# Kernel optimization log

Hardware: AMD Instinct MI355X
Metric: run time of the kernel (lower is better)

The kernel has to match this reference:

```python
import jax, jax.numpy as jnp
import numpy as np

N_NODES = 50000
N_EDGES = 800000
NFEAT = 256
NHID = 512
BN_EPS = 1e-5


def setup_inputs() -> dict:
    key = jax.random.key(0)
    ks = jax.random.split(key, 6)
    x = jax.random.normal(ks[0], (N_NODES, NFEAT), dtype=jnp.float32)
    edge_index = jax.random.randint(ks[1], (2, N_EDGES), 0, N_NODES, dtype=jnp.int64)
    # Xavier-uniform linear weights, zero biases (matches weights_init)
    lim1 = np.sqrt(6.0 / (NFEAT + NHID))
    W1 = jax.random.uniform(ks[2], (NFEAT, NHID), minval=-lim1, maxval=lim1, dtype=jnp.float32)
    b1 = jnp.zeros((NHID,), dtype=jnp.float32)
    lim2 = np.sqrt(6.0 / (NHID + NHID))
    W2 = jax.random.uniform(ks[3], (NHID, NHID), minval=-lim2, maxval=lim2, dtype=jnp.float32)
    b2 = jnp.zeros((NHID,), dtype=jnp.float32)
    gamma = jnp.ones((NHID,), dtype=jnp.float32)
    beta = jnp.zeros((NHID,), dtype=jnp.float32)
    return {"x": x, "edge_index": edge_index, "W1": W1, "b1": b1,
            "gamma": gamma, "beta": beta, "W2": W2, "b2": b2}


def reference(x, edge_index, W1, b1, gamma, beta, W2, b2):
    # GINConv (eps=0): h_i = MLP(x_i + sum_{j->i} x_j)
    src = edge_index[0]
    dst = edge_index[1]
    agg = jax.ops.segment_sum(x[src], dst, num_segments=x.shape[0])  # [N, nfeat]
    h = x + agg
    # MLP: Linear -> ReLU -> BatchNorm1d (training-mode batch stats) -> Linear
    h = jax.nn.relu(h @ W1 + b1)  # [N, nhid]
    mean = jnp.mean(h, axis=0)
    var = jnp.var(h, axis=0)  # biased, as PyTorch uses for normalization
    h = (h - mean) * jax.lax.rsqrt(var + BN_EPS) * gamma + beta
    return h @ W2 + b2
```

## Files before the change

kernel.cpp:

```cpp
#include <hip/hip_runtime.h>

#define NNODES 50000
#define NF 256
#define NH 512
#define MPAD 50048
#define NRB 391
#define BN_EPS 1e-5f
#define NSCAN 196

typedef unsigned short u16;
typedef __attribute__((ext_vector_type(8))) short bf16x8;
typedef __attribute__((ext_vector_type(4))) float f32x4;

__device__ __forceinline__ float bf2f(u16 u) {
  union { unsigned int i; float f; } v; v.i = ((unsigned int)u) << 16; return v.f;
}
__device__ __forceinline__ u16 f2bf(float f) {
  union { float ff; unsigned int i; } v; v.ff = f;
  unsigned int r = v.i + 0x7FFFu + ((v.i >> 16) & 1u);
  return (u16)(r >> 16);
}

__device__ __forceinline__ void async16(const void* g, void* l) {
  __builtin_amdgcn_global_load_lds(
      (const __attribute__((address_space(1))) unsigned int*)g,
      (__attribute__((address_space(3))) unsigned int*)l, 16, 0, 0);
}

__global__ __launch_bounds__(256) void conv_tr_kernel(const float* __restrict__ x,
                                                      u16* __restrict__ xbf,
                                                      const float* __restrict__ W1,
                                                      u16* __restrict__ W1t) {
  const int b = blockIdx.x;
  if (b < 2048) {
    const size_t n8 = (size_t)NNODES * NF / 8;
    size_t stride = (size_t)2048 * 256;
    for (size_t i = b * (size_t)256 + threadIdx.x; i < n8; i += stride) {
      float4 a = ((const float4*)x)[2 * i];
      float4 c = ((const float4*)x)[2 * i + 1];
      ushort4 lo, hi;
      lo.x = f2bf(a.x); lo.y = f2bf(a.y); lo.z = f2bf(a.z); lo.w = f2bf(a.w);
      hi.x = f2bf(c.x); hi.y = f2bf(c.y); hi.z = f2bf(c.z); hi.w = f2bf(c.w);
      ((ushort4*)xbf)[2 * i] = lo;
      ((ushort4*)xbf)[2 * i + 1] = hi;
    }
  } else {
    int idx = (b - 2048) * 256 + threadIdx.x;
    int n = idx >> 8;
    int k = idx & 255;
    W1t[(size_t)n * NF + k] = f2bf(W1[(size_t)k * NH + n]);
  }
}

__global__ __launch_bounds__(256) void hist_kernel(const int* __restrict__ ei,
                                                   int* __restrict__ deg, int E) {
  __shared__ int sf;
  if (threadIdx.x < 64) {
    unsigned long long bb = __ballot(ei[2 * threadIdx.x + 1] == 0);
    if (threadIdx.x == 0) sf = (bb == ~0ull) ? 1 : 0;
  }
  __syncthreads();
  const int is64 = sf;
  const int gtid = blockIdx.x * 256 + threadIdx.x;
  const int stride = gridDim.x * 256;
  if (is64) {
    const int4* d4 = (const int4*)(ei + 2 * (size_t)E);
    int np = E >> 1;
    for (int p = gtid; p < np; p += stride) {
      int4 d = d4[p];
      if ((unsigned)d.x < NNODES) atomicAdd(&deg[d.x], 1);
      if ((unsigned)d.z < NNODES) atomicAdd(&deg[d.z], 1);
    }
    for (int e = (np << 1) + gtid; e < E; e += stride) {
      int d = ei[2 * (size_t)E + 2 * e];
      if ((unsigned)d < NNODES) atomicAdd(&deg[d], 1);
    }
  } else {
    const int4* d4 = (const int4*)(ei + E);
    int np = E >> 2;
    for (int p = gtid; p < np; p += stride) {
      int4 d = d4[p];
      if ((unsigned)d.x < NNODES) atomicAdd(&deg[d.x], 1);
      if ((unsigned)d.y < NNODES) atomicAdd(&deg[d.y], 1);
      if ((unsigned)d.z < NNODES) atomicAdd(&deg[d.z], 1);
      if ((unsigned)d.w < NNODES) atomicAdd(&deg[d.w], 1);
    }
    for (int e = (np << 2) + gtid; e < E; e += stride) {
      int d = ei[(size_t)E + e];
      if ((unsigned)d < NNODES) atomicAdd(&deg[d], 1);
    }
  }
}

__global__ __launch_bounds__(256) void scan_a(const int* __restrict__ deg,
                                              int* __restrict__ rowptr,
                                              int* __restrict__ blocksums) {
  const int t = threadIdx.x;
  int i = blockIdx.x * 256 + t;
  int v = (i < NNODES) ? deg[i] : 0;
  __shared__ int sm[256];
  sm[t] = v;
  __syncthreads();
  for (int off = 1; off < 256; off <<= 1) {
    int u = (t >= off) ? sm[t - off] : 0;
    __syncthreads();
    sm[t] += u;
    __syncthreads();
  }
  if (i < NNODES) rowptr[i] = sm[t] - v;
  if (t == 255) blocksums[blockIdx.x] = sm[255];
}

__global__ __launch_bounds__(256) void scan_b(const int* __restrict__ blocksums,
                                              int* __restrict__ rowptr,
                                              int* __restrict__ cw) {
  const int t = threadIdx.x;
  __shared__ int sm[256];
  sm[t] = (t < NSCAN) ? blocksums[t] : 0;
  __syncthreads();
  for (int off = 1; off < 256; off <<= 1) {
    int u = (t >= off) ? sm[t - off] : 0;
    __syncthreads();
    sm[t] += u;
    __syncthreads();
  }
  const int boff = (blockIdx.x == 0) ? 0 : sm[blockIdx.x - 1];
  int i = blockIdx.x * 256 + t;
  if (i < NNODES) {
    int rv = rowptr[i] + boff;
    rowptr[i] = rv;
    cw[i] = rv;
  }
  if (blockIdx.x == 0 && t == 0) rowptr[NNODES] = sm[NSCAN - 1];
}

__global__ __launch_bounds__(256) void fill_kernel(const int* __restrict__ ei, int E,
                                                   int* __restrict__ cw,
                                                   int* __restrict__ srcs) {
  __shared__ int sf;
  if (threadIdx.x < 64) {
    unsigned long long bb = __ballot(ei[2 * threadIdx.x + 1] == 0);
    if (threadIdx.x == 0) sf = (bb == ~0ull) ? 1 : 0;
  }
  __syncthreads();
  const int is64 = sf;
  const int gtid = blockIdx.x * 256 + threadIdx.x;
  const int stride = gridDim.x * 256;
  if (is64) {
    const int4* s4 = (const int4*)ei;
    const int4* d4 = (const int4*)(ei + 2 * (size_t)E);
    int np = E >> 1;
    for (int p = gtid; p < np; p += stride) {
      int4 sv = s4[p], dv = d4[p];
      if ((unsigned)sv.x < NNODES && (unsigned)dv.x < NNODES) {
        int pos = atomicAdd(&cw[dv.x], 1);
        if ((unsigned)pos < (unsigned)E) srcs[pos] = sv.x;
      }
      if ((unsigned)sv.z < NNODES && (unsigned)dv.z < NNODES) {
        int pos = atomicAdd(&cw[dv.z], 1);
        if ((unsigned)pos < (unsigned)E) srcs[pos] = sv.z;
      }
    }
    for (int e = (np << 1) + gtid; e < E; e += stride) {
      int src = ei[2 * e], dst = ei[2 * (size_t)E + 2 * e];
      if ((unsigned)src >= NNODES || (unsigned)dst >= NNODES) continue;
      int pos = atomicAdd(&cw[dst], 1);
      if ((unsigned)pos < (unsigned)E) srcs[pos] = src;
    }
  } else {
    const int4* s4 = (const int4*)ei;
    const int4* d4 = (const int4*)(ei + E);
    int np = E >> 2;
    for (int p = gtid; p < np; p += stride) {
      int4 sv = s4[p], dv = d4[p];
      int ss[4] = {sv.x, sv.y, sv.z, sv.w};
      int dd[4] = {dv.x, dv.y, dv.z, dv.w};
#pragma unroll
      for (int j = 0; j < 4; ++j) {
        if ((unsigned)ss[j] < NNODES && (unsigned)dd[j] < NNODES) {
          int pos = atomicAdd(&cw[dd[j]], 1);
          if ((unsigned)pos < (unsigned)E) srcs[pos] = ss[j];
        }
      }
    }
    for (int e = (np << 2) + gtid; e < E; e += stride) {
      int src = ei[e], dst = ei[(size_t)E + e];
      if ((unsigned)src >= NNODES || (unsigned)dst >= NNODES) continue;
      int pos = atomicAdd(&cw[dst], 1);
      if ((unsigned)pos < (unsigned)E) srcs[pos] = src;
    }
  }
}

__global__ __launch_bounds__(256) void gather_kernel(const u16* __restrict__ xbf,
                                                     const int* __restrict__ srcs,
                                                     const int* __restrict__ rowptr,
                                                     u16* __restrict__ hpad) {
  const int hl = threadIdx.x & 31;
  const int node = blockIdx.x * 8 + (threadIdx.x >> 5);
  if (node >= MPAD) return;
  bf16x8* outp = (bf16x8*)(hpad + (size_t)node * NF + hl * 8);
  if (node >= NNODES) {
    bf16x8 z = {0, 0, 0, 0, 0, 0, 0, 0};
    *outp = z;
    return;
  }
  bf16x8 sv = *(const bf16x8*)(xbf + (size_t)node * NF + hl * 8);
  float acc[8];
#pragma unroll
  for (int j = 0; j < 8; ++j) acc[j] = bf2f((u16)sv[j]);
  int e = rowptr[node];
  const int e1 = rowptr[node + 1];
  for (; e + 7 < e1; e += 8) {
    bf16x8 v[8];
#pragma unroll
    for (int u = 0; u < 8; ++u)
      v[u] = *(const bf16x8*)(xbf + (size_t)srcs[e + u] * NF + hl * 8);
#pragma unroll
    for (int u = 0; u < 8; ++u)
#pragma unroll
      for (int j = 0; j < 8; ++j) acc[j] += bf2f((u16)v[u][j]);
  }
  for (; e + 3 < e1; e += 4) {
    bf16x8 v[4];
#pragma unroll
    for (int u = 0; u < 4; ++u)
      v[u] = *(const bf16x8*)(xbf + (size_t)srcs[e + u] * NF + hl * 8);
#pragma unroll
    for (int u = 0; u < 4; ++u)
#pragma unroll
      for (int j = 0; j < 8; ++j) acc[j] += bf2f((u16)v[u][j]);
  }
  for (; e < e1; ++e) {
    bf16x8 v0 = *(const bf16x8*)(xbf + (size_t)srcs[e] * NF + hl * 8);
#pragma unroll
    for (int j = 0; j < 8; ++j) acc[j] += bf2f((u16)v0[j]);
  }
  bf16x8 o;
#pragma unroll
  for (int j = 0; j < 8; ++j) o[j] = (short)f2bf(acc[j]);
  *outp = o;
}

template <int K, bool RELU, bool OUTF32, bool STATS>
__global__ __launch_bounds__(256) void gemm_bt(const u16* __restrict__ Ab,
                                               const u16* __restrict__ Bt,
                                               const float* __restrict__ bias,
                                               void* __restrict__ Cp, int Mstore,
                                               float* __restrict__ parts) {
  __shared__ __align__(16) u16 As[128 * 64];
  __shared__ __align__(16) u16 Bs[128 * 64];
  __shared__ float sred[256];
  const int tid = threadIdx.x;
  const int lane = tid & 63;
  const int wid = tid >> 6;
  const int wr = wid >> 1, wc = wid & 1;

  const int nwg = gridDim.x;
  const int q = nwg >> 3, r = nwg & 7;
  const int xcd = blockIdx.x & 7, idx = blockIdx.x >> 3;
  const int work = (xcd < r ? xcd * (q + 1) : r * (q + 1) + (xcd - r) * q) + idx;
  const int brow = (work >> 2) * 128;
  const int bcol = (work & 3) * 128;

  f32x4 acc[4][4] = {};

  const int lrow = lane >> 3;
  const int lkc = ((lane & 7) ^ (lrow & 7)) * 8;
  const int nt = K / 64;

  if (STATS) {
    if (tid < 64) ((float4*)sred)[tid] = (float4){0.f, 0.f, 0.f, 0.f};
  }

  for (int t = 0; t < nt; ++t) {
    const int k0 = t * 64;
#pragma unroll
    for (int i = 0; i < 4; ++i) {
      int c = i * 4 + wid;
      int row = c * 8 + lrow;
      async16(Ab + (size_t)(brow + row) * K + k0 + lkc, &As[c * 512]);
      async16(Bt + (size_t)(bcol + row) * K + k0 + lkc, &Bs[c * 512]);
    }
    __syncthreads();
#pragma unroll
    for (int ks = 0; ks < 2; ++ks) {
      bf16x8 af[4], bfr[4];
      const int rchunk = ((ks << 2) + (lane >> 4)) ^ (lane & 7);
#pragma unroll
      for (int m = 0; m < 4; ++m)
        af[m] = *(const bf16x8*)&As[(wr * 64 + m * 16 + (lane & 15)) * 64 + rchunk * 8];
#pragma unroll
      for (int n = 0; n < 4; ++n)
        bfr[n] = *(const bf16x8*)&Bs[(wc * 64 + n * 16 + (lane & 15)) * 64 + rchunk * 8];
#pragma unroll
      for (int n = 0; n < 4; ++n)
#pragma unroll
        for (int m = 0; m < 4; ++m)
          acc[n][m] = __builtin_amdgcn_mfma_f32_16x16x32_bf16(bfr[n], af[m], acc[n][m], 0, 0, 0);
    }
    __syncthreads();
  }

  const int row_base = brow + wr * 64 + (lane & 15);
  const int col_base = bcol + wc * 64 + ((lane >> 4) << 2);
#pragma unroll
  for (int n = 0; n < 4; ++n) {
    int col = col_base + n * 16;
    float4 bv4 = *(const float4*)&bias[col];
    float s0 = 0.f, s1 = 0.f, s2 = 0.f, s3 = 0.f;
    float q0 = 0.f, q1 = 0.f, q2 = 0.f, q3 = 0.f;
#pragma unroll
    for (int m = 0; m < 4; ++m) {
      int row = row_base + m * 16;
      f32x4 a = acc[n][m];
      float v0 = a[0] + bv4.x, v1 = a[1] + bv4.y, v2 = a[2] + bv4.z, v3 = a[3] + bv4.w;
      if (RELU) {
        v0 = fmaxf(v0, 0.f); v1 = fmaxf(v1, 0.f);
        v2 = fmaxf(v2, 0.f); v3 = fmaxf(v3, 0.f);
      }
      if (row < Mstore) {
        if (OUTF32) {
          float4 o = {v0, v1, v2, v3};
          *(float4*)&((float*)Cp)[(size_t)row * NH + col] = o;
        } else {
          ushort4 o = {f2bf(v0), f2bf(v1), f2bf(v2), f2bf(v3)};
          *(ushort4*)&((u16*)Cp)[(size_t)row * NH + col] = o;
        }
      }
      if (STATS && row < NNODES) {
        s0 += v0; s1 += v1; s2 += v2; s3 += v3;
        q0 += v0 * v0; q1 += v1 * v1; q2 += v2 * v2; q3 += v3 * v3;
      }
    }
    if (STATS) {
#pragma unroll
      for (int msk = 1; msk < 16; msk <<= 1) {
        s0 += __shfl_xor(s0, msk); s1 += __shfl_xor(s1, msk);
        s2 += __shfl_xor(s2, msk); s3 += __shfl_xor(s3, msk);
        q0 += __shfl_xor(q0, msk); q1 += __shfl_xor(q1, msk);
        q2 += __shfl_xor(q2, msk); q3 += __shfl_xor(q3, msk);
      }
      if ((lane & 15) == 0) {
        int lc = wc * 64 + n * 16 + ((lane >> 4) << 2);
        atomicAdd(&sred[lc + 0], s0); atomicAdd(&sred[lc + 1], s1);
        atomicAdd(&sred[lc + 2], s2); atomicAdd(&sred[lc + 3], s3);
        atomicAdd(&sred[128 + lc + 0], q0); atomicAdd(&sred[128 + lc + 1], q1);
        atomicAdd(&sred[128 + lc + 2], q2); atomicAdd(&sred[128 + lc + 3], q3);
      }
    }
  }
  if (STATS) {
    __syncthreads();
    if (tid < 128) {
      parts[(size_t)work * 256 + tid] = sred[tid];
      parts[(size_t)work * 256 + 128 + tid] = sred[128 + tid];
    }
  }
}

__global__ __launch_bounds__(256) void stats_bn(const float* __restrict__ parts,
                                                const float* __restrict__ gamma,
                                                const float* __restrict__ beta,
                                                float* __restrict__ a_arr,
                                                float* __restrict__ c_arr,
                                                int* __restrict__ err) {
  int c = blockIdx.x * 256 + threadIdx.x;
  int grp = (c >> 7) & 3, cl = c & 127;
  float s = 0.f, qq = 0.f;
  for (int rb = 0; rb < NRB; ++rb) {
    const float* p = parts + (size_t)((rb << 2) + grp) * 256 + cl;
    s += p[0];
    qq += p[128];
  }
  float mean = s * (1.f / NNODES);
  float var = qq * (1.f / NNODES) - mean * mean;
  if (!(mean == mean) || !(var == var) ||
      fabsf(mean) > 1e20f || var > 1e20f || var < -1e-2f)
    err[0] = 2;
  if (var < 0.f) var = 0.f;
  float a = gamma[c] * rsqrtf(var + BN_EPS);
  a_arr[c] = a;
  c_arr[c] = beta[c] - mean * a;
}

__global__ __launch_bounds__(256) void fold_w2(const float* __restrict__ W2,
                                               const float* __restrict__ b2,
                                               const float* __restrict__ a_arr,
                                               const float* __restrict__ c_arr,
                                               u16* __restrict__ W2pt,
                                               float* __restrict__ bias2p) {
  int n = blockIdx.x;
  int t = threadIdx.x;
  float accv = 0.f;
  for (int k = t; k < NH; k += 256) {
    float w = W2[(size_t)k * NH + n];
    W2pt[(size_t)n * NH + k] = f2bf(a_arr[k] * w);
    accv += c_arr[k] * w;
  }
  __shared__ float red[256];
  red[t] = accv;
  __syncthreads();
  for (int s = 128; s > 0; s >>= 1) {
    if (t < s) red[t] += red[t + s];
    __syncthreads();
  }
  if (t == 0) bias2p[n] = b2[n] + red[0];
}

__global__ __launch_bounds__(256) void write_sentinel(float* __restrict__ out, int n, float val) {
  int stride = gridDim.x * blockDim.x;
  for (int i = blockIdx.x * blockDim.x + threadIdx.x; i < n; i += stride) out[i] = val;
}

__global__ __launch_bounds__(256) void apply_err(const int* __restrict__ err,
                                                 float* __restrict__ out, int n) {
  if (err[0] == 0) return;
  int stride = gridDim.x * blockDim.x;
  for (int i = blockIdx.x * blockDim.x + threadIdx.x; i < n; i += stride) out[i] = -500000.f;
}

extern "C" void kernel_launch(void* const* d_in, const int* in_sizes, int n_in,
                              void* d_out, int out_size, void* d_ws, size_t ws_size,
                              hipStream_t stream) {
  const float* x     = (const float*)d_in[0];
  const int*   ei    = (const int*)d_in[1];
  const float* W1    = (const float*)d_in[2];
  const float* b1    = (const float*)d_in[3];
  const float* gamma = (const float*)d_in[4];
  const float* beta  = (const float*)d_in[5];
  const float* W2    = (const float*)d_in[6];
  const float* b2    = (const float*)d_in[7];
  float* out = (float*)d_out;
  const int E = in_sizes[1] / 2;

  char* ws = (char*)d_ws;
  size_t off = 0;
  auto alloc = [&](size_t bytes) {
    char* p = ws + off;
    off += (bytes + 255) & ~(size_t)255;
    return p;
  };
  u16*   xbf    = (u16*)alloc((size_t)NNODES * NF * 2);
  u16*   hpad   = (u16*)alloc((size_t)MPAD * NF * 2);
  u16*   h1     = (u16*)alloc((size_t)MPAD * NH * 2);
  u16*   W1t    = (u16*)alloc((size_t)NH * NF * 2);
  u16*   W2pt   = (u16*)alloc((size_t)NH * NH * 2);
  int*   srcs   = (int*)alloc((size_t)E * 4);
  int*   rowptr = (int*)alloc((size_t)(NNODES + 1) * 4);
  int*   cw     = (int*)alloc((size_t)NNODES * 4);
  int*   deg    = (int*)alloc((size_t)NNODES * 4);
  int*   bsums  = (int*)alloc(256 * 4);
  float* parts  = (float*)alloc((size_t)NRB * 4 * 256 * 4);
  int*   err    = (int*)alloc(8);
  float* a_arr  = (float*)alloc(NH * 4);
  float* c_arr  = (float*)alloc(NH * 4);
  float* bias2p = (float*)alloc(NH * 4);

  if (off > ws_size) {
    write_sentinel<<<2048, 256, 0, stream>>>(out, out_size,
        1.0e7f + 1048576.0f * (float)(ws_size >> 20));
    return;
  }

  hipMemsetAsync(deg, 0, (size_t)NNODES * 4, stream);
  hipMemsetAsync(err, 0, 8, stream);

  hist_kernel<<<1024, 256, 0, stream>>>(ei, deg, E);
  conv_tr_kernel<<<2560, 256, 0, stream>>>(x, xbf, W1, W1t);
  scan_a<<<NSCAN, 256, 0, stream>>>(deg, rowptr, bsums);
  scan_b<<<NSCAN, 256, 0, stream>>>(bsums, rowptr, cw);
  fill_kernel<<<1024, 256, 0, stream>>>(ei, E, cw, srcs);
  gather_kernel<<<MPAD / 8, 256, 0, stream>>>(xbf, srcs, rowptr, hpad);

  const int nwg = NRB * 4;
  gemm_bt<NF, true, false, true><<<nwg, 256, 0, stream>>>(hpad, W1t, b1, h1, MPAD, parts);

  stats_bn<<<2, 256, 0, stream>>>(parts, gamma, beta, a_arr, c_arr, err);
  fold_w2<<<NH, 256, 0, stream>>>(W2, b2, a_arr, c_arr, W2pt, bias2p);

  gemm_bt<NH, false, true, false><<<nwg, 256, 0, stream>>>(h1, W2pt, bias2p, out, NNODES, nullptr);

  apply_err<<<2048, 256, 0, stream>>>(err, out, out_size);
}
```

Before: 281.8 us.

## Replace CSR build with fixed-capacity per-node edge buckets

Removes the degree histogram and two prefix-scan kernels by scattering each edge source directly into a per-destination bucket of fixed capacity, with counts kept in the atomic cursor array. The gather kernel reads the bucket count and list directly instead of row pointers. This cuts several launches and one full pass over the edge list, at the cost of a larger, sparsely filled index buffer. An error flag is raised if any node exceeds the capacity.

```diff
diff --git a/kernel.cpp b/kernel.cpp
--- a/kernel.cpp
+++ b/kernel.cpp
@@ -6,7 +6,7 @@
 #define MPAD 50048
 #define NRB 391
 #define BN_EPS 1e-5f
-#define NSCAN 196
+#define CAP 96
 
 typedef unsigned short u16;
 typedef __attribute__((ext_vector_type(8))) short bf16x8;
@@ -52,91 +52,10 @@
   }
 }
 
-__global__ __launch_bounds__(256) void hist_kernel(const int* __restrict__ ei,
-                                                   int* __restrict__ deg, int E) {
-  __shared__ int sf;
-  if (threadIdx.x < 64) {
-    unsigned long long bb = __ballot(ei[2 * threadIdx.x + 1] == 0);
-    if (threadIdx.x == 0) sf = (bb == ~0ull) ? 1 : 0;
-  }
-  __syncthreads();
-  const int is64 = sf;
-  const int gtid = blockIdx.x * 256 + threadIdx.x;
-  const int stride = gridDim.x * 256;
-  if (is64) {
-    const int4* d4 = (const int4*)(ei + 2 * (size_t)E);
-    int np = E >> 1;
-    for (int p = gtid; p < np; p += stride) {
-      int4 d = d4[p];
-      if ((unsigned)d.x < NNODES) atomicAdd(&deg[d.x], 1);
-      if ((unsigned)d.z < NNODES) atomicAdd(&deg[d.z], 1);
-    }
-    for (int e = (np << 1) + gtid; e < E; e += stride) {
-      int d = ei[2 * (size_t)E + 2 * e];
-      if ((unsigned)d < NNODES) atomicAdd(&deg[d], 1);
-    }
-  } else {
-    const int4* d4 = (const int4*)(ei + E);
-    int np = E >> 2;
-    for (int p = gtid; p < np; p += stride) {
-      int4 d = d4[p];
-      if ((unsigned)d.x < NNODES) atomicAdd(&deg[d.x], 1);
-      if ((unsigned)d.y < NNODES) atomicAdd(&deg[d.y], 1);
-      if ((unsigned)d.z < NNODES) atomicAdd(&deg[d.z], 1);
-      if ((unsigned)d.w < NNODES) atomicAdd(&deg[d.w], 1);
-    }
-    for (int e = (np << 2) + gtid; e < E; e += stride) {
-      int d = ei[(size_t)E + e];
-      if ((unsigned)d < NNODES) atomicAdd(&deg[d], 1);
-    }
-  }
-}
-
-__global__ __launch_bounds__(256) void scan_a(const int* __restrict__ deg,
-                                              int* __restrict__ rowptr,
-                                              int* __restrict__ blocksums) {
-  const int t = threadIdx.x;
-  int i = blockIdx.x * 256 + t;
-  int v = (i < NNODES) ? deg[i] : 0;
-  __shared__ int sm[256];
-  sm[t] = v;
-  __syncthreads();
-  for (int off = 1; off < 256; off <<= 1) {
-    int u = (t >= off) ? sm[t - off] : 0;
-    __syncthreads();
-    sm[t] += u;
-    __syncthreads();
-  }
-  if (i < NNODES) rowptr[i] = sm[t] - v;
-  if (t == 255) blocksums[blockIdx.x] = sm[255];
-}
-
-__global__ __launch_bounds__(256) void scan_b(const int* __restrict__ blocksums,
-                                              int* __restrict__ rowptr,
-                                              int* __restrict__ cw) {
-  const int t = threadIdx.x;
-  __shared__ int sm[256];
-  sm[t] = (t < NSCAN) ? blocksums[t] : 0;
-  __syncthreads();
-  for (int off = 1; off < 256; off <<= 1) {
-    int u = (t >= off) ? sm[t - off] : 0;
-    __syncthreads();
-    sm[t] += u;
-    __syncthreads();
-  }
-  const int boff = (blockIdx.x == 0) ? 0 : sm[blockIdx.x - 1];
-  int i = blockIdx.x * 256 + t;
-  if (i < NNODES) {
-    int rv = rowptr[i] + boff;
-    rowptr[i] = rv;
-    cw[i] = rv;
-  }
-  if (blockIdx.x == 0 && t == 0) rowptr[NNODES] = sm[NSCAN - 1];
-}
-
-__global__ __launch_bounds__(256) void fill_kernel(const int* __restrict__ ei, int E,
+__global__ __launch_bounds__(256) void bucket_fill(const int* __restrict__ ei, int E,
                                                    int* __restrict__ cw,
-                                                   int* __restrict__ srcs) {
+                                                   int* __restrict__ srcs,
+                                                   int* __restrict__ err) {
   __shared__ int sf;
   if (threadIdx.x < 64) {
     unsigned long long bb = __ballot(ei[2 * threadIdx.x + 1] == 0);
@@ -154,18 +73,18 @@
       int4 sv = s4[p], dv = d4[p];
       if ((unsigned)sv.x < NNODES && (unsigned)dv.x < NNODES) {
         int pos = atomicAdd(&cw[dv.x], 1);
-        if ((unsigned)pos < (unsigned)E) srcs[pos] = sv.x;
+        if (pos < CAP) srcs[(size_t)dv.x * CAP + pos] = sv.x; else err[0] = 4;
       }
       if ((unsigned)sv.z < NNODES && (unsigned)dv.z < NNODES) {
         int pos = atomicAdd(&cw[dv.z], 1);
-        if ((unsigned)pos < (unsigned)E) srcs[pos] = sv.z;
+        if (pos < CAP) srcs[(size_t)dv.z * CAP + pos] = sv.z; else err[0] = 4;
       }
     }
     for (int e = (np << 1) + gtid; e < E; e += stride) {
       int src = ei[2 * e], dst = ei[2 * (size_t)E + 2 * e];
       if ((unsigned)src >= NNODES || (unsigned)dst >= NNODES) continue;
       int pos = atomicAdd(&cw[dst], 1);
-      if ((unsigned)pos < (unsigned)E) srcs[pos] = src;
+      if (pos < CAP) srcs[(size_t)dst * CAP + pos] = src; else err[0] = 4;
     }
   } else {
     const int4* s4 = (const int4*)ei;
@@ -179,7 +98,7 @@
       for (int j = 0; j < 4; ++j) {
         if ((unsigned)ss[j] < NNODES && (unsigned)dd[j] < NNODES) {
           int pos = atomicAdd(&cw[dd[j]], 1);
-          if ((unsigned)pos < (unsigned)E) srcs[pos] = ss[j];
+          if (pos < CAP) srcs[(size_t)dd[j] * CAP + pos] = ss[j]; else err[0] = 4;
         }
       }
     }
@@ -187,14 +106,14 @@
       int src = ei[e], dst = ei[(size_t)E + e];
       if ((unsigned)src >= NNODES || (unsigned)dst >= NNODES) continue;
       int pos = atomicAdd(&cw[dst], 1);
-      if ((unsigned)pos < (unsigned)E) srcs[pos] = src;
+      if (pos < CAP) srcs[(size_t)dst * CAP + pos] = src; else err[0] = 4;
     }
   }
 }
 
 __global__ __launch_bounds__(256) void gather_kernel(const u16* __restrict__ xbf,
                                                      const int* __restrict__ srcs,
-                                                     const int* __restrict__ rowptr,
+                                                     const int* __restrict__ cw,
                                                      u16* __restrict__ hpad) {
   const int hl = threadIdx.x & 31;
   const int node = blockIdx.x * 8 + (threadIdx.x >> 5);
@@ -209,30 +128,22 @@
   float acc[8];
 #pragma unroll
   for (int j = 0; j < 8; ++j) acc[j] = bf2f((u16)sv[j]);
-  int e = rowptr[node];
-  const int e1 = rowptr[node + 1];
-  for (; e + 7 < e1; e += 8) {
-    bf16x8 v[8];
-#pragma unroll
-    for (int u = 0; u < 8; ++u)
-      v[u] = *(const bf16x8*)(xbf + (size_t)srcs[e + u] * NF + hl * 8);
-#pragma unroll
-    for (int u = 0; u < 8; ++u)
+  int cnt = cw[node];
+  if (cnt > CAP) cnt = CAP;
+  const int* lst = srcs + (size_t)node * CAP;
+  int e = 0;
+  for (; e + 3 < cnt; e += 4) {
+    bf16x8 v[4];
+#pragma unroll
+    for (int u = 0; u < 4; ++u)
+      v[u] = *(const bf16x8*)(xbf + (size_t)lst[e + u] * NF + hl * 8);
+#pragma unroll
+    for (int u = 0; u < 4; ++u)
 #pragma unroll
       for (int j = 0; j < 8; ++j) acc[j] += bf2f((u16)v[u][j]);
   }
-  for (; e + 3 < e1; e += 4) {
-    bf16x8 v[4];
-#pragma unroll
-    for (int u = 0; u < 4; ++u)
-      v[u] = *(const bf16x8*)(xbf + (size_t)srcs[e + u] * NF + hl * 8);
-#pragma unroll
-    for (int u = 0; u < 4; ++u)
-#pragma unroll
-      for (int j = 0; j < 8; ++j) acc[j] += bf2f((u16)v[u][j]);
-  }
-  for (; e < e1; ++e) {
-    bf16x8 v0 = *(const bf16x8*)(xbf + (size_t)srcs[e] * NF + hl * 8);
+  for (; e < cnt; ++e) {
+    bf16x8 v0 = *(const bf16x8*)(xbf + (size_t)lst[e] * NF + hl * 8);
 #pragma unroll
     for (int j = 0; j < 8; ++j) acc[j] += bf2f((u16)v0[j]);
   }
@@ -446,11 +357,8 @@
   u16*   h1     = (u16*)alloc((size_t)MPAD * NH * 2);
   u16*   W1t    = (u16*)alloc((size_t)NH * NF * 2);
   u16*   W2pt   = (u16*)alloc((size_t)NH * NH * 2);
-  int*   srcs   = (int*)alloc((size_t)E * 4);
-  int*   rowptr = (int*)alloc((size_t)(NNODES + 1) * 4);
+  int*   srcs   = (int*)alloc((size_t)NNODES * CAP * 4);
   int*   cw     = (int*)alloc((size_t)NNODES * 4);
-  int*   deg    = (int*)alloc((size_t)NNODES * 4);
-  int*   bsums  = (int*)alloc(256 * 4);
   float* parts  = (float*)alloc((size_t)NRB * 4 * 256 * 4);
   int*   err    = (int*)alloc(8);
   float* a_arr  = (float*)alloc(NH * 4);
@@ -463,15 +371,12 @@
     return;
   }
 
-  hipMemsetAsync(deg, 0, (size_t)NNODES * 4, stream);
+  hipMemsetAsync(cw, 0, (size_t)NNODES * 4, stream);
   hipMemsetAsync(err, 0, 8, stream);
 
-  hist_kernel<<<1024, 256, 0, stream>>>(ei, deg, E);
+  bucket_fill<<<1024, 256, 0, stream>>>(ei, E, cw, srcs, err);
   conv_tr_kernel<<<2560, 256, 0, stream>>>(x, xbf, W1, W1t);
-  scan_a<<<NSCAN, 256, 0, stream>>>(deg, rowptr, bsums);
-  scan_b<<<NSCAN, 256, 0, stream>>>(bsums, rowptr, cw);
-  fill_kernel<<<1024, 256, 0, stream>>>(ei, E, cw, srcs);
-  gather_kernel<<<MPAD / 8, 256, 0, stream>>>(xbf, srcs, rowptr, hpad);
+  gather_kernel<<<MPAD / 8, 256, 0, stream>>>(xbf, srcs, cw, hpad);
 
   const int nwg = NRB * 4;
   gemm_bt<NF, true, false, true><<<nwg, 256, 0, stream>>>(hpad, W1t, b1, h1, MPAD, parts);
```

New measurement: 234.6 us. -16.8%, faster.
